# Performance work log

Hardware: AMD Instinct MI355X
Metric: run time of the kernel (lower is better)

## Reference

```python
import jax, jax.numpy as jnp
import numpy as np


def setup_inputs() -> dict:
    key = jax.random.key(0)
    ks = jax.random.split(key, 7)
    batch, hidden, k = 16384, 1024, 16
    return {
        "A": jax.random.normal(ks[0], (batch, hidden), dtype=jnp.float32),
        "B": jax.random.normal(ks[1], (batch, hidden), dtype=jnp.float32),
        "W": jax.random.normal(ks[2], (k, hidden, hidden), dtype=jnp.float32),
        "V_w": jax.random.normal(ks[3], (k, 2 * hidden), dtype=jnp.float32) * 0.02,
        "V_b": jax.random.normal(ks[4], (k,), dtype=jnp.float32) * 0.02,
        "out_w": jax.random.normal(ks[5], (1, k), dtype=jnp.float32) * 0.02,
        "out_b": jax.random.normal(ks[6], (1,), dtype=jnp.float32) * 0.02,
    }


def reference(A, B, W, V_w, V_b, out_b, out_w):
    # Bilinear tensor scores: score[b,i] = sum_d (A @ W[i])[b,d] * B[b,d]
    # Batched over k instead of the original python loop.
    AW = jnp.einsum("bh,khd->bkd", A, W)          # [batch, k, hidden]
    tensor_scores = jnp.einsum("bkd,bd->bk", AW, B)  # [batch, k]
    # Linear fusion on concatenated pair features.
    linear = jnp.concatenate([A, B], axis=1) @ V_w.T + V_b  # [batch, k]
    h = jnp.tanh(tensor_scores + linear)
    return (h @ out_w.T + out_b).squeeze(-1)  # [batch]
```

## Files before the change

kernel.cpp:

```cpp
#include <hip/hip_runtime.h>
#include <hip/hip_bf16.h>
#include <stdint.h>

typedef __bf16 bf16x8 __attribute__((ext_vector_type(8)));
typedef float  f32x4  __attribute__((ext_vector_type(4)));

#define BATCH 16384
#define HID   1024
#define KK    16
#define NKB   32
#define BM    128
#define BN    128

__device__ __forceinline__ unsigned short bf16_rne(float x) {
    uint32_t u = __float_as_uint(x);
    uint32_t r = (u + 0x7fffu + ((u >> 16) & 1u)) >> 16;
    return (unsigned short)r;
}
__device__ __forceinline__ void split2(float x, unsigned short& h, unsigned short& l) {
    h = bf16_rne(x);
    float hf = __uint_as_float(((uint32_t)h) << 16);
    l = bf16_rne(x - hf);
}

__global__ __launch_bounds__(256) void k_split_a(const float* __restrict__ A,
                                                 unsigned short* __restrict__ Acomb) {
    uint32_t q   = blockIdx.x * 256u + threadIdx.x;
    uint32_t b   = q >> 8;
    uint32_t rem = q & 255u;
    uint32_t kb  = rem >> 3;
    uint32_t j   = (rem & 7u) * 4u;
    float4 v = *(const float4*)(A + (size_t)b * HID + kb * 32 + j);
    ushort4 hi, lo;
    split2(v.x, hi.x, lo.x); split2(v.y, hi.y, lo.y);
    split2(v.z, hi.z, lo.z); split2(v.w, hi.w, lo.w);
    unsigned short* dst = Acomb + ((size_t)kb * BATCH + b) * 64 + j;
    *(ushort4*)(dst)      = hi;
    *(ushort4*)(dst + 32) = lo;
}

__global__ __launch_bounds__(256) void k_split_w(const float* __restrict__ W,
                                                 unsigned short* __restrict__ Wcomb) {
    int bx = blockIdx.x;
    int i  = bx >> 9;
    int kb = (bx >> 4) & 31;
    int dt = bx & 15;
    __shared__ float lds[32][65];
    const float* src = W + ((size_t)i * HID + (size_t)kb * 32) * HID + dt * 64;
    int t = threadIdx.x;
    #pragma unroll
    for (int rep = 0; rep < 8; ++rep) {
        int lin = rep * 256 + t;
        int hl = lin >> 6, dl = lin & 63;
        lds[hl][dl] = src[(size_t)hl * HID + dl];
    }
    __syncthreads();
    #pragma unroll
    for (int rep = 0; rep < 2; ++rep) {
        int cid = rep * 256 + t;
        int dl = cid >> 3, qq = cid & 7;
        unsigned short outv[8];
        #pragma unroll
        for (int j = 0; j < 8; ++j) {
            int col = qq * 8 + j;
            float x = (col < 32) ? lds[col][dl] : lds[col - 32][dl];
            unsigned short h, l; split2(x, h, l);
            outv[j] = (col < 32) ? h : l;
        }
        *(uint4*)(Wcomb + ((((size_t)i * NKB + kb) * HID) + dt * 64 + dl) * 64 + qq * 8)
            = *(uint4*)outv;
    }
}

__global__ __launch_bounds__(256, 2) void k_gemm(const unsigned short* __restrict__ Acomb,
                                                 const unsigned short* __restrict__ Wcomb,
                                                 const float* __restrict__ B,
                                                 float* __restrict__ score) {
    __shared__ __align__(16) unsigned short ldsA[BM * 64];
    __shared__ __align__(16) unsigned short ldsW[BN * 64];
    const int tid  = threadIdx.x;
    const int lane = tid & 63;
    const int wave = tid >> 6;
    const int wm = wave >> 1, wn = wave & 1;
    const int brow = blockIdx.x * BM;
    const int dcol = blockIdx.y * BN;
    const int i    = blockIdx.z;
    const int l15 = lane & 15, l4 = lane >> 4;

    f32x4 acc[4][4];
    #pragma unroll
    for (int m = 0; m < 4; ++m)
        #pragma unroll
        for (int n = 0; n < 4; ++n)
            acc[m][n] = (f32x4){0.f, 0.f, 0.f, 0.f};

    const unsigned short* baseA = Acomb + (size_t)brow * 64;
    const unsigned short* baseW = Wcomb + ((size_t)i * NKB * HID + dcol) * 64;

    int aoff_h[4], aoff_l[4], woff_h[4], woff_l[4];
    #pragma unroll
    for (int m = 0; m < 4; ++m) {
        int row = wm * 64 + m * 16 + l15;
        aoff_h[m] = row * 64 + ((l4    ) ^ (row & 7)) * 8;
        aoff_l[m] = row * 64 + ((l4 + 4) ^ (row & 7)) * 8;
    }
    #pragma unroll
    for (int n = 0; n < 4; ++n) {
        int row = wn * 64 + n * 16 + l15;
        woff_h[n] = row * 64 + ((l4    ) ^ (row & 7)) * 8;
        woff_l[n] = row * 64 + ((l4 + 4) ^ (row & 7)) * 8;
    }

    for (int kb = 0; kb < NKB; ++kb) {
        const unsigned short* srcA = baseA + (size_t)kb * ((size_t)BATCH * 64);
        const unsigned short* srcW = baseW + (size_t)kb * ((size_t)HID * 64);
        #pragma unroll
        for (int r = 0; r < 4; ++r) {
            int c = r * 256 + tid;
            int row = c >> 3, sl = c & 7;
            uint4 va = *(const uint4*)(srcA + c * 8);
            uint4 vw = *(const uint4*)(srcW + c * 8);
            int sw = sl ^ (row & 7);
            *(uint4*)(&ldsA[row * 64 + sw * 8]) = va;
            *(uint4*)(&ldsW[row * 64 + sw * 8]) = vw;
        }
        __syncthreads();
        bf16x8 ah[4], al[4], wh[4], wl[4];
        #pragma unroll
        for (int m = 0; m < 4; ++m) {
            ah[m] = *(const bf16x8*)(&ldsA[aoff_h[m]]);
            al[m] = *(const bf16x8*)(&ldsA[aoff_l[m]]);
        }
        #pragma unroll
        for (int n = 0; n < 4; ++n) {
            wh[n] = *(const bf16x8*)(&ldsW[woff_h[n]]);
            wl[n] = *(const bf16x8*)(&ldsW[woff_l[n]]);
        }
        #pragma unroll
        for (int m = 0; m < 4; ++m)
            #pragma unroll
            for (int n = 0; n < 4; ++n) {
                acc[m][n] = __builtin_amdgcn_mfma_f32_16x16x32_bf16(ah[m], wh[n], acc[m][n], 0, 0, 0);
                acc[m][n] = __builtin_amdgcn_mfma_f32_16x16x32_bf16(ah[m], wl[n], acc[m][n], 0, 0, 0);
                acc[m][n] = __builtin_amdgcn_mfma_f32_16x16x32_bf16(al[m], wh[n], acc[m][n], 0, 0, 0);
            }
        __syncthreads();
    }

    #pragma unroll
    for (int m = 0; m < 4; ++m) {
        #pragma unroll
        for (int r = 0; r < 4; ++r) {
            int row = brow + wm * 64 + m * 16 + l4 * 4 + r;
            float s = 0.f;
            #pragma unroll
            for (int n = 0; n < 4; ++n) {
                int col = dcol + wn * 64 + n * 16 + l15;
                s += acc[m][n][r] * B[(size_t)row * HID + col];
            }
            s += __shfl_xor(s, 1);
            s += __shfl_xor(s, 2);
            s += __shfl_xor(s, 4);
            s += __shfl_xor(s, 8);
            if (l15 == 0) atomicAdd(&score[(size_t)row * KK + i], s);
        }
    }
}

__global__ __launch_bounds__(256) void k_linear(const float* __restrict__ A,
                                                const float* __restrict__ B,
                                                const float* __restrict__ Vw,
                                                const float* __restrict__ Vb,
                                                float* __restrict__ lin) {
    __shared__ float4 sA[128][9];
    __shared__ float4 sB[128][9];
    __shared__ float4 sVa[16][9];
    __shared__ float4 sVb[16][9];
    const int t = threadIdx.x;
    const int brow = blockIdx.x * 128;
    const int b_loc = t >> 1;
    const int ihalf = t & 1;
    float acc8[8] = {0.f, 0.f, 0.f, 0.f, 0.f, 0.f, 0.f, 0.f};

    for (int hc = 0; hc < HID; hc += 32) {
        __syncthreads();
        #pragma unroll
        for (int rep = 0; rep < 4; ++rep) {
            int idx = rep * 256 + t;
            int bl = idx >> 3, h4 = idx & 7;
            sA[bl][h4] = *(const float4*)(A + (size_t)(brow + bl) * HID + hc + h4 * 4);
            sB[bl][h4] = *(const float4*)(B + (size_t)(brow + bl) * HID + hc + h4 * 4);
        }
        if (t < 128) {
            int ii = t >> 3, h4 = t & 7;
            sVa[ii][h4] = *(const float4*)(Vw + (size_t)ii * 2048 + hc + h4 * 4);
        } else {
            int tt = t - 128;
            int ii = tt >> 3, h4 = tt & 7;
            sVb[ii][h4] = *(const float4*)(Vw + (size_t)ii * 2048 + 1024 + hc + h4 * 4);
        }
        __syncthreads();
        #pragma unroll
        for (int h4 = 0; h4 < 8; ++h4) {
            float4 a4 = sA[b_loc][h4];
            float4 b4 = sB[b_loc][h4];
            #pragma unroll
            for (int ii = 0; ii < 8; ++ii) {
                int iG = ihalf * 8 + ii;
                float4 va = sVa[iG][h4], vb = sVb[iG][h4];
                acc8[ii] += a4.x * va.x + a4.y * va.y + a4.z * va.z + a4.w * va.w
                          + b4.x * vb.x + b4.y * vb.y + b4.z * vb.z + b4.w * vb.w;
            }
        }
    }
    #pragma unroll
    for (int ii = 0; ii < 8; ++ii) {
        int iG = ihalf * 8 + ii;
        lin[(size_t)(brow + b_loc) * KK + iG] = acc8[ii] + Vb[iG];
    }
}

__global__ __launch_bounds__(256) void k_final(const float* __restrict__ score,
                                               const float* __restrict__ lin,
                                               const float* __restrict__ out_w,
                                               const float* __restrict__ out_b,
                                               float* __restrict__ out) {
    int b = blockIdx.x * 256 + threadIdx.x;
    float o = out_b[0];
    #pragma unroll
    for (int i = 0; i < KK; ++i)
        o += out_w[i] * tanhf(score[(size_t)b * KK + i] + lin[(size_t)b * KK + i]);
    out[b] = o;
}

extern "C" void kernel_launch(void* const* d_in, const int* in_sizes, int n_in,
                              void* d_out, int out_size, void* d_ws, size_t ws_size,
                              hipStream_t stream) {
    (void)in_sizes; (void)n_in; (void)out_size; (void)ws_size;
    const float* A     = (const float*)d_in[0];
    const float* B     = (const float*)d_in[1];
    const float* W     = (const float*)d_in[2];
    const float* Vw    = (const float*)d_in[3];
    const float* Vb    = (const float*)d_in[4];
    const float* out_w = (const float*)d_in[5];
    const float* out_b = (const float*)d_in[6];
    float* out = (float*)d_out;

    unsigned short* Acomb = (unsigned short*)d_ws;
    unsigned short* Wcomb = Acomb + (size_t)NKB * BATCH * 64;
    float* score = (float*)(Wcomb + (size_t)KK * NKB * HID * 64);
    float* lin   = score + (size_t)BATCH * KK;

    hipMemsetAsync(score, 0, (size_t)BATCH * KK * sizeof(float), stream);
    k_split_a<<<dim3(16384), dim3(256), 0, stream>>>(A, Acomb);
    k_split_w<<<dim3(8192), dim3(256), 0, stream>>>(W, Wcomb);
    dim3 g(BATCH / BM, HID / BN, KK);
    k_gemm<<<g, dim3(256), 0, stream>>>(Acomb, Wcomb, B, score);
    k_linear<<<dim3(BATCH / 128), dim3(256), 0, stream>>>(A, B, Vw, Vb, lin);
    k_final<<<dim3(BATCH / 256), dim3(256), 0, stream>>>(score, lin, out_w, out_b, out);
}
```

Baseline: 1.901 ms.

## Double-buffer GEMM with direct global-to-LDS loads and 256x256 tiles

Rewrites the bilinear GEMM to use 256x256 tiles with 512 threads and double-buffered LDS. Global data is loaded straight into LDS with global_load_lds, so the next k-block is fetched while MFMAs run on the current one. The XOR swizzle now happens in the split kernels' global layout, which lets the async copies be contiguous. MFMA phases run at raised wave priority, with barriers in between. This targets load latency and the register round trip, and improves reuse per tile. In exchange it uses 128KB of LDS per block, has a larger accumulator register footprint, and creates fewer blocks.

```diff
diff --git a/kernel.cpp b/kernel.cpp
--- a/kernel.cpp
+++ b/kernel.cpp
@@ -4,13 +4,16 @@
 
 typedef __bf16 bf16x8 __attribute__((ext_vector_type(8)));
 typedef float  f32x4  __attribute__((ext_vector_type(4)));
+typedef unsigned short ushort_t;
 
 #define BATCH 16384
 #define HID   1024
 #define KK    16
 #define NKB   32
-#define BM    128
-#define BN    128
+#define BM    256
+#define BN    256
+#define BUFS  32768
+#define LDSW_OFF 16384
 
 __device__ __forceinline__ unsigned short bf16_rne(float x) {
     uint32_t u = __float_as_uint(x);
@@ -24,23 +27,28 @@
 }
 
 __global__ __launch_bounds__(256) void k_split_a(const float* __restrict__ A,
-                                                 unsigned short* __restrict__ Acomb) {
+                                                 ushort_t* __restrict__ Acomb) {
     uint32_t q   = blockIdx.x * 256u + threadIdx.x;
-    uint32_t b   = q >> 8;
-    uint32_t rem = q & 255u;
-    uint32_t kb  = rem >> 3;
-    uint32_t j   = (rem & 7u) * 4u;
-    float4 v = *(const float4*)(A + (size_t)b * HID + kb * 32 + j);
-    ushort4 hi, lo;
-    split2(v.x, hi.x, lo.x); split2(v.y, hi.y, lo.y);
-    split2(v.z, hi.z, lo.z); split2(v.w, hi.w, lo.w);
-    unsigned short* dst = Acomb + ((size_t)kb * BATCH + b) * 64 + j;
-    *(ushort4*)(dst)      = hi;
-    *(ushort4*)(dst + 32) = lo;
+    uint32_t b   = q >> 7;
+    uint32_t rem = q & 127u;
+    uint32_t kb  = rem >> 2;
+    uint32_t cq  = rem & 3u;
+    const float* src = A + (size_t)b * HID + kb * 32 + cq * 8;
+    float4 v0 = *(const float4*)src;
+    float4 v1 = *(const float4*)(src + 4);
+    ushort_t h[8], l[8];
+    split2(v0.x, h[0], l[0]); split2(v0.y, h[1], l[1]);
+    split2(v0.z, h[2], l[2]); split2(v0.w, h[3], l[3]);
+    split2(v1.x, h[4], l[4]); split2(v1.y, h[5], l[5]);
+    split2(v1.z, h[6], l[6]); split2(v1.w, h[7], l[7]);
+    ushort_t* row = Acomb + ((size_t)kb * BATCH + b) * 64;
+    uint32_t sw = b & 7u;
+    *(uint4*)(row + ((cq      ) ^ sw) * 8) = *(uint4*)h;
+    *(uint4*)(row + ((cq + 4u) ^ sw) * 8) = *(uint4*)l;
 }
 
 __global__ __launch_bounds__(256) void k_split_w(const float* __restrict__ W,
-                                                 unsigned short* __restrict__ Wcomb) {
+                                                 ushort_t* __restrict__ Wcomb) {
     int bx = blockIdx.x;
     int i  = bx >> 9;
     int kb = (bx >> 4) & 31;
@@ -59,7 +67,7 @@
     for (int rep = 0; rep < 2; ++rep) {
         int cid = rep * 256 + t;
         int dl = cid >> 3, qq = cid & 7;
-        unsigned short outv[8];
+        ushort_t outv[8];
         #pragma unroll
         for (int j = 0; j < 8; ++j) {
             int col = qq * 8 + j;
@@ -67,97 +75,133 @@
             unsigned short h, l; split2(x, h, l);
             outv[j] = (col < 32) ? h : l;
         }
-        *(uint4*)(Wcomb + ((((size_t)i * NKB + kb) * HID) + dt * 64 + dl) * 64 + qq * 8)
-            = *(uint4*)outv;
-    }
-}
-
-__global__ __launch_bounds__(256, 2) void k_gemm(const unsigned short* __restrict__ Acomb,
-                                                 const unsigned short* __restrict__ Wcomb,
+        *(uint4*)(Wcomb + ((((size_t)i * NKB + kb) * HID) + dt * 64 + dl) * 64
+                  + (qq ^ (dl & 7)) * 8) = *(uint4*)outv;
+    }
+}
+
+#define BAR() asm volatile("s_barrier" ::: "memory")
+#define GLL(gsrc, dstIdx) \
+    __builtin_amdgcn_global_load_lds((const __attribute__((address_space(1))) void*)(gsrc), \
+        (__attribute__((address_space(3))) void*)(&smem[(dstIdx)]), 16, 0, 0)
+
+__global__ __launch_bounds__(512, 2) void k_gemm(const ushort_t* __restrict__ Acomb,
+                                                 const ushort_t* __restrict__ Wcomb,
                                                  const float* __restrict__ B,
                                                  float* __restrict__ score) {
-    __shared__ __align__(16) unsigned short ldsA[BM * 64];
-    __shared__ __align__(16) unsigned short ldsW[BN * 64];
+    __shared__ __align__(16) ushort_t smem[2 * BUFS];
     const int tid  = threadIdx.x;
     const int lane = tid & 63;
     const int wave = tid >> 6;
-    const int wm = wave >> 1, wn = wave & 1;
+    const int wm = wave >> 2, wn = wave & 3;
+    const int l15 = lane & 15, l4 = lane >> 4;
     const int brow = blockIdx.x * BM;
     const int dcol = blockIdx.y * BN;
     const int i    = blockIdx.z;
-    const int l15 = lane & 15, l4 = lane >> 4;
-
-    f32x4 acc[4][4];
-    #pragma unroll
-    for (int m = 0; m < 4; ++m)
+
+    f32x4 acc[8][4];
+    #pragma unroll
+    for (int m = 0; m < 8; ++m)
         #pragma unroll
         for (int n = 0; n < 4; ++n)
             acc[m][n] = (f32x4){0.f, 0.f, 0.f, 0.f};
 
-    const unsigned short* baseA = Acomb + (size_t)brow * 64;
-    const unsigned short* baseW = Wcomb + ((size_t)i * NKB * HID + dcol) * 64;
-
-    int aoff_h[4], aoff_l[4], woff_h[4], woff_l[4];
-    #pragma unroll
-    for (int m = 0; m < 4; ++m) {
-        int row = wm * 64 + m * 16 + l15;
-        aoff_h[m] = row * 64 + ((l4    ) ^ (row & 7)) * 8;
-        aoff_l[m] = row * 64 + ((l4 + 4) ^ (row & 7)) * 8;
-    }
-    #pragma unroll
-    for (int n = 0; n < 4; ++n) {
-        int row = wn * 64 + n * 16 + l15;
-        woff_h[n] = row * 64 + ((l4    ) ^ (row & 7)) * 8;
-        woff_l[n] = row * 64 + ((l4 + 4) ^ (row & 7)) * 8;
-    }
-
-    for (int kb = 0; kb < NKB; ++kb) {
-        const unsigned short* srcA = baseA + (size_t)kb * ((size_t)BATCH * 64);
-        const unsigned short* srcW = baseW + (size_t)kb * ((size_t)HID * 64);
+    const int csw_hi = ((l4    ) ^ (l15 & 7)) * 8;
+    const int csw_lo = ((l4 + 4) ^ (l15 & 7)) * 8;
+    const int aoff_hi = (wm * 128 + l15) * 64 + csw_hi;
+    const int aoff_lo = (wm * 128 + l15) * 64 + csw_lo;
+    const int woff_hi = LDSW_OFF + (wn * 64 + l15) * 64 + csw_hi;
+    const int woff_lo = LDSW_OFF + (wn * 64 + l15) * 64 + csw_lo;
+
+    const ushort_t* gA0 = Acomb + ((size_t)brow + wave * 16) * 64 + lane * 8;
+    const ushort_t* gW0 = Wcomb + ((size_t)i * NKB * HID + dcol + wave * 16) * 64 + lane * 8;
+    const int sdst = wave * 1024;
+
+#define STAGE_A(c, t1, h) do { \
+    const ushort_t* g_ = gA0 + ((size_t)(t1) * BATCH + (h) * 128) * 64; \
+    GLL(g_,       (c) * BUFS + (h) * 8192 + sdst); \
+    GLL(g_ + 512, (c) * BUFS + (h) * 8192 + sdst + 512); \
+  } while (0)
+#define STAGE_W(c, t1, h) do { \
+    const ushort_t* g_ = gW0 + ((size_t)(t1) * HID + (h) * 128) * 64; \
+    GLL(g_,       (c) * BUFS + LDSW_OFF + (h) * 8192 + sdst); \
+    GLL(g_ + 512, (c) * BUFS + LDSW_OFF + (h) * 8192 + sdst + 512); \
+  } while (0)
+
+    bf16x8 ah[4], al[4], wh[4], wl[4];
+#define RD_W(n, cb) do { \
+    wh[n] = *(const bf16x8*)(&smem[(cb) + woff_hi + (n) * 1024]); \
+    wl[n] = *(const bf16x8*)(&smem[(cb) + woff_lo + (n) * 1024]); } while (0)
+#define RD_A(m, slot, cb) do { \
+    ah[slot] = *(const bf16x8*)(&smem[(cb) + aoff_hi + (m) * 1024]); \
+    al[slot] = *(const bf16x8*)(&smem[(cb) + aoff_lo + (m) * 1024]); } while (0)
+
+#define MFMA_Q(MB, NB) do { \
+    __builtin_amdgcn_s_setprio(1); \
+    _Pragma("unroll") \
+    for (int mm = 0; mm < 4; ++mm) { \
+      _Pragma("unroll") \
+      for (int nn = 0; nn < 2; ++nn) \
+        acc[(MB)+mm][(NB)+nn] = __builtin_amdgcn_mfma_f32_16x16x32_bf16(ah[mm], wh[(NB)+nn], acc[(MB)+mm][(NB)+nn], 0, 0, 0); } \
+    _Pragma("unroll") \
+    for (int mm = 0; mm < 4; ++mm) { \
+      _Pragma("unroll") \
+      for (int nn = 0; nn < 2; ++nn) \
+        acc[(MB)+mm][(NB)+nn] = __builtin_amdgcn_mfma_f32_16x16x32_bf16(ah[mm], wl[(NB)+nn], acc[(MB)+mm][(NB)+nn], 0, 0, 0); } \
+    _Pragma("unroll") \
+    for (int mm = 0; mm < 4; ++mm) { \
+      _Pragma("unroll") \
+      for (int nn = 0; nn < 2; ++nn) \
+        acc[(MB)+mm][(NB)+nn] = __builtin_amdgcn_mfma_f32_16x16x32_bf16(al[mm], wh[(NB)+nn], acc[(MB)+mm][(NB)+nn], 0, 0, 0); } \
+    __builtin_amdgcn_s_setprio(0); \
+  } while (0)
+
+#define TILE_BODY(c, t, DOSTAGE) do { \
+    const int cb = (c) * BUFS; \
+     \
+    if (DOSTAGE) { STAGE_A((c) ^ 1, (t) + 1, 0); STAGE_A((c) ^ 1, (t) + 1, 1); } \
+    RD_W(0, cb); RD_W(1, cb); \
+    RD_A(0, 0, cb); RD_A(1, 1, cb); RD_A(2, 2, cb); RD_A(3, 3, cb); \
+    BAR(); \
+    MFMA_Q(0, 0); \
+    BAR(); \
+     \
+    if (DOSTAGE) { STAGE_W((c) ^ 1, (t) + 1, 0); STAGE_W((c) ^ 1, (t) + 1, 1); } \
+    RD_W(2, cb); RD_W(3, cb); \
+    BAR(); \
+    MFMA_Q(0, 2); \
+    BAR(); \
+     \
+    RD_A(4, 0, cb); RD_A(5, 1, cb); RD_A(6, 2, cb); RD_A(7, 3, cb); \
+    BAR(); \
+    MFMA_Q(4, 0); \
+    BAR(); \
+     \
+    MFMA_Q(4, 2); \
+    __syncthreads(); \
+  } while (0)
+
+    STAGE_A(0, 0, 0); STAGE_A(0, 0, 1);
+    STAGE_W(0, 0, 0); STAGE_W(0, 0, 1);
+    __syncthreads();
+
+    int cur = 0;
+    for (int t = 0; t < NKB - 1; ++t) {
+        TILE_BODY(cur, t, 1);
+        cur ^= 1;
+    }
+    TILE_BODY(cur, NKB - 1, 0);
+
+    #pragma unroll
+    for (int m = 0; m < 8; ++m) {
         #pragma unroll
         for (int r = 0; r < 4; ++r) {
-            int c = r * 256 + tid;
-            int row = c >> 3, sl = c & 7;
-            uint4 va = *(const uint4*)(srcA + c * 8);
-            uint4 vw = *(const uint4*)(srcW + c * 8);
-            int sw = sl ^ (row & 7);
-            *(uint4*)(&ldsA[row * 64 + sw * 8]) = va;
-            *(uint4*)(&ldsW[row * 64 + sw * 8]) = vw;
-        }
-        __syncthreads();
-        bf16x8 ah[4], al[4], wh[4], wl[4];
-        #pragma unroll
-        for (int m = 0; m < 4; ++m) {
-            ah[m] = *(const bf16x8*)(&ldsA[aoff_h[m]]);
-            al[m] = *(const bf16x8*)(&ldsA[aoff_l[m]]);
-        }
-        #pragma unroll
-        for (int n = 0; n < 4; ++n) {
-            wh[n] = *(const bf16x8*)(&ldsW[woff_h[n]]);
-            wl[n] = *(const bf16x8*)(&ldsW[woff_l[n]]);
-        }
-        #pragma unroll
-        for (int m = 0; m < 4; ++m)
-            #pragma unroll
-            for (int n = 0; n < 4; ++n) {
-                acc[m][n] = __builtin_amdgcn_mfma_f32_16x16x32_bf16(ah[m], wh[n], acc[m][n], 0, 0, 0);
-                acc[m][n] = __builtin_amdgcn_mfma_f32_16x16x32_bf16(ah[m], wl[n], acc[m][n], 0, 0, 0);
-                acc[m][n] = __builtin_amdgcn_mfma_f32_16x16x32_bf16(al[m], wh[n], acc[m][n], 0, 0, 0);
-            }
-        __syncthreads();
-    }
-
-    #pragma unroll
-    for (int m = 0; m < 4; ++m) {
-        #pragma unroll
-        for (int r = 0; r < 4; ++r) {
-            int row = brow + wm * 64 + m * 16 + l4 * 4 + r;
-            float s = 0.f;
-            #pragma unroll
-            for (int n = 0; n < 4; ++n) {
-                int col = dcol + wn * 64 + n * 16 + l15;
-                s += acc[m][n][r] * B[(size_t)row * HID + col];
-            }
+            int row = brow + wm * 128 + m * 16 + l4 * 4 + r;
+            const float* Brow = B + (size_t)row * HID + dcol + wn * 64 + l15;
+            float s = acc[m][0][r] * Brow[0]
+                    + acc[m][1][r] * Brow[16]
+                    + acc[m][2][r] * Brow[32]
+                    + acc[m][3][r] * Brow[48];
             s += __shfl_xor(s, 1);
             s += __shfl_xor(s, 2);
             s += __shfl_xor(s, 4);
@@ -246,16 +290,15 @@
     const float* out_b = (const float*)d_in[6];
     float* out = (float*)d_out;
 
-    unsigned short* Acomb = (unsigned short*)d_ws;
-    unsigned short* Wcomb = Acomb + (size_t)NKB * BATCH * 64;
+    ushort_t* Acomb = (ushort_t*)d_ws;
+    ushort_t* Wcomb = Acomb + (size_t)NKB * BATCH * 64;
     float* score = (float*)(Wcomb + (size_t)KK * NKB * HID * 64);
     float* lin   = score + (size_t)BATCH * KK;
 
     hipMemsetAsync(score, 0, (size_t)BATCH * KK * sizeof(float), stream);
-    k_split_a<<<dim3(16384), dim3(256), 0, stream>>>(A, Acomb);
+    k_split_a<<<dim3(8192), dim3(256), 0, stream>>>(A, Acomb);
     k_split_w<<<dim3(8192), dim3(256), 0, stream>>>(W, Wcomb);
-    dim3 g(BATCH / BM, HID / BN, KK);
-    k_gemm<<<g, dim3(256), 0, stream>>>(Acomb, Wcomb, B, score);
+    k_gemm<<<dim3(BATCH / BM, HID / BN, KK), dim3(512), 0, stream>>>(Acomb, Wcomb, B, score);
     k_linear<<<dim3(BATCH / 128), dim3(256), 0, stream>>>(A, B, Vw, Vb, lin);
     k_final<<<dim3(BATCH / 256), dim3(256), 0, stream>>>(score, lin, out_w, out_b, out);
 }
```

New measurement: 1.647 ms. 13.4% less time.
